# Performance work log

Measured on AMD Instinct MI355X. Metric: run time of the kernel, lower is better.

## Reference

```python
import jax, jax.numpy as jnp
import numpy as np

D_MODEL = 64
NODES = 325
TOPK = 8
HEADS = 4
D_INNER = 2 * D_MODEL      # mamba_ssm default expand=2
D_STATE = 16               # mamba_ssm default
D_CONV = 4                 # mamba_ssm default
DT_RANK = 4                # ceil(d_model/16)
B_SZ, T_LEN = 8, 64
EPS = 1e-5


def _layernorm(x, g, b):
    m = jnp.mean(x, -1, keepdims=True)
    v = jnp.mean(jnp.square(x - m), -1, keepdims=True)
    return (x - m) * jax.lax.rsqrt(v + EPS) * g + b


def _mamba(h, in_proj_w, conv_w, conv_b, x_proj_w, dt_w, dt_b, A_log, D_ssm, out_w):
    # h: (BN, T, D_MODEL)
    BN, T, _ = h.shape
    xz = h @ in_proj_w.T                      # (BN,T,2*di)
    xi, z = jnp.split(xz, 2, axis=-1)
    # depthwise causal conv1d, kernel D_CONV (unrolled: tiny fixed loop)
    xp = jnp.pad(xi, ((0, 0), (D_CONV - 1, 0), (0, 0)))
    xc = conv_b + sum(xp[:, j:j + T, :] * conv_w[:, j] for j in range(D_CONV))
    xc = jax.nn.silu(xc)
    dbl = xc @ x_proj_w.T                     # (BN,T,dt_rank+2*ds)
    dt = dbl[..., :DT_RANK]
    Bc = dbl[..., DT_RANK:DT_RANK + D_STATE]
    Cc = dbl[..., DT_RANK + D_STATE:]
    dt = jax.nn.softplus(dt @ dt_w.T + dt_b)  # (BN,T,di)
    A = -jnp.exp(A_log)                       # (di,ds)

    def step(hs, inp):
        dt_t, B_t, C_t, x_t = inp             # (BN,di),(BN,ds),(BN,ds),(BN,di)
        dA = jnp.exp(dt_t[..., None] * A)     # (BN,di,ds)
        hs = hs * dA + (dt_t * x_t)[..., None] * B_t[:, None, :]
        y = jnp.einsum('bds,bs->bd', hs, C_t)
        return hs, y

    tm = lambda a: jnp.swapaxes(a, 0, 1)      # time-major for scan
    h0 = jnp.zeros((BN, D_INNER, D_STATE), xc.dtype)
    _, ys = jax.lax.scan(step, h0, (tm(dt), tm(Bc), tm(Cc), tm(xc)))
    y = tm(ys) + D_ssm * xc
    y = y * jax.nn.silu(z)
    return y @ out_w.T


def setup_inputs() -> dict:
    key = jax.random.key(0)
    ks = jax.random.split(key, 24)
    rn = lambda k, s, sc=0.05: jax.random.normal(k, s, jnp.float32) * sc
    inp = {}
    inp['x'] = jax.random.normal(ks[0], (B_SZ, T_LEN, NODES, D_MODEL), jnp.float32)
    adj = jax.random.normal(ks[1], (NODES, NODES), jnp.float32)
    _, nbr = jax.lax.top_k(adj, TOPK)
    inp['neighbor_idx'] = nbr.astype(jnp.int32)           # (N, k) static buffer
    # temporal block
    inp['ln1_g'] = jnp.ones((D_MODEL,)); inp['ln1_b'] = jnp.zeros((D_MODEL,))
    inp['in_proj_w'] = rn(ks[2], (2 * D_INNER, D_MODEL))
    inp['conv_w'] = rn(ks[3], (D_INNER, D_CONV), 0.2)
    inp['conv_b'] = jnp.zeros((D_INNER,))
    inp['x_proj_w'] = rn(ks[4], (DT_RANK + 2 * D_STATE, D_INNER))
    inp['dt_w'] = rn(ks[5], (D_INNER, DT_RANK), 0.5)
    inp['dt_b'] = rn(ks[6], (D_INNER,), 0.5)
    inp['A_log'] = jnp.log(jnp.tile(jnp.arange(1, D_STATE + 1, dtype=jnp.float32), (D_INNER, 1)))
    inp['D_ssm'] = jnp.ones((D_INNER,))
    inp['out_w'] = rn(ks[7], (D_MODEL, D_INNER))
    # sparse graph attention
    for nm, k in (('q', 8), ('k', 9), ('v', 10), ('o', 11)):
        inp[nm + '_w'] = rn(ks[k], (D_MODEL, D_MODEL))
        inp[nm + '_b'] = jnp.zeros((D_MODEL,))
    # adaptive gate (final bias init -2.0 per module)
    inp['g1_w'] = rn(ks[12], (D_MODEL // 4, D_MODEL))
    inp['g1_b'] = jnp.zeros((D_MODEL // 4,))
    inp['g2_w'] = rn(ks[13], (1, D_MODEL // 4))
    inp['g2_b'] = jnp.full((1,), -2.0, jnp.float32)
    inp['ln2_g'] = jnp.ones((D_MODEL,)); inp['ln2_b'] = jnp.zeros((D_MODEL,))
    return inp


def reference(x, neighbor_idx, ln1_g, ln1_b, in_proj_w, conv_w, conv_b, x_proj_w,
              dt_w, dt_b, A_log, D_ssm, out_w, q_w, q_b, k_w, k_b, v_w, v_b,
              o_w, o_b, g1_w, g1_b, g2_w, g2_b, ln2_g, ln2_b):
    B, T, N, Dm = x.shape
    # --- temporal Mamba with pre-norm residual (dropout = identity, eval) ---
    xt = x.transpose(0, 2, 1, 3).reshape(B * N, T, Dm)
    xt = xt + _mamba(_layernorm(xt, ln1_g, ln1_b), in_proj_w, conv_w, conv_b,
                     x_proj_w, dt_w, dt_b, A_log, D_ssm, out_w)
    xT = xt.reshape(B, N, T, Dm).transpose(0, 2, 1, 3)     # (B,T,N,D)
    # --- sparse top-k neighbor attention ---
    hd = Dm // HEADS
    Q = (xT @ q_w.T + q_b).reshape(B, T, N, HEADS, hd)
    K = (xT @ k_w.T + k_b).reshape(B, T, N, HEADS, hd)
    V = (xT @ v_w.T + v_b).reshape(B, T, N, HEADS, hd)
    Kn = K[:, :, neighbor_idx]                 # (B,T,N,k,H,hd)
    Vn = V[:, :, neighbor_idx]
    attn = jnp.einsum('btnhd,btnkhd->btnhk', Q, Kn) * (hd ** -0.5)
    attn = jax.nn.softmax(attn, axis=-1)
    og = jnp.einsum('btnhk,btnkhd->btnhd', attn, Vn).reshape(B, T, N, Dm)
    x_graph = og @ o_w.T + o_b
    # --- adaptive gate + fusion + final norm ---
    g = jax.nn.sigmoid(jax.nn.gelu(xT @ g1_w.T + g1_b, approximate=False) @ g2_w.T + g2_b)
    out = xT + g * (x_graph - xT)
    return _layernorm(out, ln2_g, ln2_b)
```

## Files before the change

kernel.cpp:

```cpp
#include <hip/hip_runtime.h>
#include <math.h>

#define NODES   325
#define TOPK    8
#define B_SZ    8
#define T_LEN   64
#define EPS     1e-5f
#define NTOK    ((size_t)B_SZ * T_LEN * NODES)

#define WPAD    132
#define OWPAD   68
#define XCPAD   132
#define DBLPAD  40
#define OFF_H   0
#define OFF_XC  4096
#define OFF_DBL 12544
#define OFF_DTV 15104
#define OFF_W   23296
#define SMEM_BYTES ((23296+8704)*4)

__device__ __forceinline__ float waveSum64(float v){
  #pragma unroll
  for(int m=1;m<64;m<<=1) v += __shfl_xor(v, m, 64);
  return v;
}
__device__ __forceinline__ float groupSum16(float v){
  v += __shfl_xor(v, 1, 64);
  v += __shfl_xor(v, 2, 64);
  v += __shfl_xor(v, 4, 64);
  v += __shfl_xor(v, 8, 64);
  return v;
}
__device__ __forceinline__ float dot64(const float* __restrict__ s,
                                       const float* __restrict__ w, float acc){
  #pragma unroll
  for(int q=0;q<64;q++) acc = fmaf(s[q], w[q], acc);
  return acc;
}
__device__ __forceinline__ float4 f4fma(float s, float4 a, float4 acc){
  acc.x = fmaf(s, a.x, acc.x);
  acc.y = fmaf(s, a.y, acc.y);
  acc.z = fmaf(s, a.z, acc.z);
  acc.w = fmaf(s, a.w, acc.w);
  return acc;
}
__device__ __forceinline__ float dp4(float4 a, float4 b, float acc){
  acc = fmaf(a.x, b.x, acc);
  acc = fmaf(a.y, b.y, acc);
  acc = fmaf(a.z, b.z, acc);
  acc = fmaf(a.w, b.w, acc);
  return acc;
}

__global__ __launch_bounds__(512)
void opt_mamba(const float* __restrict__ x,
               const float* __restrict__ ln1_g, const float* __restrict__ ln1_b,
               const float* __restrict__ in_w,
               const float* __restrict__ conv_w, const float* __restrict__ conv_b,
               const float* __restrict__ xp_w,
               const float* __restrict__ dt_w, const float* __restrict__ dt_b,
               const float* __restrict__ A_log, const float* __restrict__ Dss,
               const float* __restrict__ out_w,
               float* __restrict__ xT)
{
  extern __shared__ float sm[];
  float* s_h   = sm + OFF_H;
  float* s_xc  = sm + OFF_XC;
  float* s_dbl = sm + OFF_DBL;
  float* s_dtv = sm + OFF_DTV;
  float* sW    = sm + OFF_W;

  const int bn   = blockIdx.x;
  const int b    = bn / NODES;
  const int n    = bn % NODES;
  const int tid  = threadIdx.x;
  const int lane = tid & 63;
  const int wv   = tid >> 6;

  const int r0 = (tid & 31) * 4;
  const int t0 = (tid >> 5) * 4;

  for(int idx = tid; idx < 128*64; idx += 512){
    int r = idx >> 6, c = idx & 63;
    sW[c*WPAD + r] = in_w[idx];
  }
  {
    const float g_ln = ln1_g[lane], b_ln = ln1_b[lane];
    #pragma unroll
    for(int i=0;i<8;i++){
      int t = wv*8 + i;
      size_t tok = (size_t)(b*T_LEN + t)*NODES + n;
      float v   = x[tok*64 + lane];
      float m   = waveSum64(v) * (1.f/64.f);
      float c   = v - m;
      float var = waveSum64(c*c) * (1.f/64.f);
      s_h[t*64 + lane] = c * rsqrtf(var + EPS) * g_ln + b_ln;
    }
  }
  __syncthreads();

  {
    float4 acc[4];
    #pragma unroll
    for(int tt=0;tt<4;tt++) acc[tt] = make_float4(0.f,0.f,0.f,0.f);
    for(int c0=0;c0<64;c0+=4){
      float4 w0 = *(const float4*)&sW[(c0+0)*WPAD + r0];
      float4 w1 = *(const float4*)&sW[(c0+1)*WPAD + r0];
      float4 w2 = *(const float4*)&sW[(c0+2)*WPAD + r0];
      float4 w3 = *(const float4*)&sW[(c0+3)*WPAD + r0];
      #pragma unroll
      for(int tt=0;tt<4;tt++){
        float4 h4 = *(const float4*)&s_h[(t0+tt)*64 + c0];
        acc[tt] = f4fma(h4.x, w0, acc[tt]);
        acc[tt] = f4fma(h4.y, w1, acc[tt]);
        acc[tt] = f4fma(h4.z, w2, acc[tt]);
        acc[tt] = f4fma(h4.w, w3, acc[tt]);
      }
    }
    #pragma unroll
    for(int tt=0;tt<4;tt++)
      *(float4*)&s_xc[(t0+tt)*XCPAD + r0] = acc[tt];
  }
  __syncthreads();

  {
    const int dd = tid & 127, tg = tid >> 7;
    float p3 = 0.f, p2 = 0.f, p1 = 0.f;
    if(tg){
      int tq = tg*16;
      p3 = s_xc[(tq-3)*XCPAD + dd];
      p2 = s_xc[(tq-2)*XCPAD + dd];
      p1 = s_xc[(tq-1)*XCPAD + dd];
    }
    __syncthreads();
    const float cw0 = conv_w[dd*4+0], cw1 = conv_w[dd*4+1];
    const float cw2 = conv_w[dd*4+2], cw3 = conv_w[dd*4+3];
    const float cb  = conv_b[dd];
    for(int t=tg*16; t<tg*16+16; t++){
      float xi = s_xc[t*XCPAD + dd];
      float v  = cb + cw0*p3 + cw1*p2 + cw2*p1 + cw3*xi;
      p3 = p2; p2 = p1; p1 = xi;
      s_xc[t*XCPAD + dd] = v / (1.f + __expf(-v));
    }
    for(int idx = tid; idx < 128*64; idx += 512){
      int r = idx >> 6, c = idx & 63;
      sW[c*WPAD + r] = in_w[128*64 + idx];
    }
  }
  __syncthreads();

  float4 zr[4];
  {
    #pragma unroll
    for(int tt=0;tt<4;tt++) zr[tt] = make_float4(0.f,0.f,0.f,0.f);
    for(int c0=0;c0<64;c0+=4){
      float4 w0 = *(const float4*)&sW[(c0+0)*WPAD + r0];
      float4 w1 = *(const float4*)&sW[(c0+1)*WPAD + r0];
      float4 w2 = *(const float4*)&sW[(c0+2)*WPAD + r0];
      float4 w3 = *(const float4*)&sW[(c0+3)*WPAD + r0];
      #pragma unroll
      for(int tt=0;tt<4;tt++){
        float4 h4 = *(const float4*)&s_h[(t0+tt)*64 + c0];
        zr[tt] = f4fma(h4.x, w0, zr[tt]);
        zr[tt] = f4fma(h4.y, w1, zr[tt]);
        zr[tt] = f4fma(h4.z, w2, zr[tt]);
        zr[tt] = f4fma(h4.w, w3, zr[tt]);
      }
    }
  }

  {
    const int td = tid & 63, rg = tid >> 6;
    const int base = rg*5;
    float dacc[5];
    #pragma unroll
    for(int i=0;i<5;i++) dacc[i] = 0.f;
    for(int c0=0;c0<128;c0+=4){
      float4 xc4 = *(const float4*)&s_xc[td*XCPAD + c0];
      #pragma unroll
      for(int i=0;i<5;i++){
        if(base+i < 36){
          float4 w4 = *(const float4*)&xp_w[(base+i)*128 + c0];
          dacc[i] = dp4(xc4, w4, dacc[i]);
        }
      }
    }
    #pragma unroll
    for(int i=0;i<5;i++)
      if(base+i < 36) s_dbl[td*DBLPAD + base + i] = dacc[i];
  }
  __syncthreads();

  {
    const int d = tid & 127, tq = tid >> 7;
    const float dtw0 = dt_w[d*4+0], dtw1 = dt_w[d*4+1];
    const float dtw2 = dt_w[d*4+2], dtw3 = dt_w[d*4+3];
    const float dtb  = dt_b[d];
    #pragma unroll
    for(int j=0;j<16;j++){
      int t = tq + j*4;
      const float* db = &s_dbl[t*DBLPAD];
      float dtv = dtb;
      dtv = fmaf(db[0], dtw0, dtv);
      dtv = fmaf(db[1], dtw1, dtv);
      dtv = fmaf(db[2], dtw2, dtv);
      dtv = fmaf(db[3], dtw3, dtv);
      dtv = fmaxf(dtv, 0.f) + log1pf(__expf(-fabsf(dtv)));
      s_dtv[t*128 + d] = dtv;
    }
  }
  __syncthreads();

  if(tid < 128){
    const int d = tid;
    float A_d[16], hs[16];
    #pragma unroll
    for(int s=0;s<16;s++){ A_d[s] = -__expf(A_log[d*16+s]); hs[s] = 0.f; }
    const float Dd = Dss[d];
    for(int t=0;t<T_LEN;t++){
      const float* db = &s_dbl[t*DBLPAD];
      float dtv = s_dtv[t*128 + d];
      float xc  = s_xc[t*XCPAD + d];
      float dx  = dtv * xc;
      float y   = 0.f;
      #pragma unroll
      for(int s=0;s<16;s++){
        float dA = __expf(dtv * A_d[s]);
        hs[s] = fmaf(dx, db[4+s], hs[s]*dA);
        y     = fmaf(hs[s], db[20+s], y);
      }
      s_xc[t*XCPAD + d] = y + Dd*xc;
    }
  }
  __syncthreads();

  {
    #pragma unroll
    for(int tt=0;tt<4;tt++){
      float4 y4 = *(const float4*)&s_xc[(t0+tt)*XCPAD + r0];
      float4 z4 = zr[tt];
      float4 u;
      u.x = y4.x * (z4.x / (1.f + __expf(-z4.x)));
      u.y = y4.y * (z4.y / (1.f + __expf(-z4.y)));
      u.z = y4.z * (z4.z / (1.f + __expf(-z4.z)));
      u.w = y4.w * (z4.w / (1.f + __expf(-z4.w)));
      *(float4*)&s_xc[(t0+tt)*XCPAD + r0] = u;
    }
    for(int idx = tid; idx < 64*128; idx += 512){
      int j = idx >> 7, c = idx & 127;
      sW[c*OWPAD + j] = out_w[idx];
    }
  }
  __syncthreads();

  {
    const int j0  = (tid & 15) * 4;
    const int t0o = (tid >> 4) * 2;
    float4 oacc[2];
    #pragma unroll
    for(int tt=0;tt<2;tt++) oacc[tt] = make_float4(0.f,0.f,0.f,0.f);
    for(int c0=0;c0<128;c0+=4){
      float4 w0 = *(const float4*)&sW[(c0+0)*OWPAD + j0];
      float4 w1 = *(const float4*)&sW[(c0+1)*OWPAD + j0];
      float4 w2 = *(const float4*)&sW[(c0+2)*OWPAD + j0];
      float4 w3 = *(const float4*)&sW[(c0+3)*OWPAD + j0];
      #pragma unroll
      for(int tt=0;tt<2;tt++){
        float4 u4 = *(const float4*)&s_xc[(t0o+tt)*XCPAD + c0];
        oacc[tt] = f4fma(u4.x, w0, oacc[tt]);
        oacc[tt] = f4fma(u4.y, w1, oacc[tt]);
        oacc[tt] = f4fma(u4.z, w2, oacc[tt]);
        oacc[tt] = f4fma(u4.w, w3, oacc[tt]);
      }
    }
    #pragma unroll
    for(int tt=0;tt<2;tt++){
      int t = t0o + tt;
      size_t tok = (size_t)(b*T_LEN + t)*NODES + n;
      float4 xv = *(const float4*)&x[tok*64 + j0];
      float4 o;
      o.x = xv.x + oacc[tt].x;
      o.y = xv.y + oacc[tt].y;
      o.z = xv.z + oacc[tt].z;
      o.w = xv.w + oacc[tt].w;
      *(float4*)&xT[tok*64 + j0] = o;
    }
  }
}

__global__ __launch_bounds__(256)
void opt_proj(const float* __restrict__ xT,
              const float* __restrict__ k_w, const float* __restrict__ k_b,
              const float* __restrict__ v_w, const float* __restrict__ v_b,
              const float* __restrict__ g1_w, const float* __restrict__ g1_b,
              const float* __restrict__ g2_w, const float* __restrict__ g2_b,
              float* __restrict__ Kb, float* __restrict__ Vb,
              float* __restrict__ gate)
{
  __shared__ float s_x[64*68];
  const int tid = threadIdx.x;
  const size_t tb = (size_t)blockIdx.x * 64;

  for(int i = tid; i < 64*64; i += 256){
    int t = i >> 6, c = i & 63;
    s_x[t*68 + c] = xT[(tb + t)*64 + c];
  }
  __syncthreads();

  const int r0 = (tid & 15) * 4;
  const int t0 = (tid >> 4) * 4;

  {
    float4 b4 = *(const float4*)&k_b[r0];
    float4 acc[4];
    #pragma unroll
    for(int tt=0;tt<4;tt++) acc[tt] = b4;
    for(int c0=0;c0<64;c0+=4){
      float4 w0 = *(const float4*)&k_w[(r0+0)*64 + c0];
      float4 w1 = *(const float4*)&k_w[(r0+1)*64 + c0];
      float4 w2 = *(const float4*)&k_w[(r0+2)*64 + c0];
      float4 w3 = *(const float4*)&k_w[(r0+3)*64 + c0];
      #pragma unroll
      for(int tt=0;tt<4;tt++){
        float4 x4 = *(const float4*)&s_x[(t0+tt)*68 + c0];
        acc[tt].x = dp4(x4, w0, acc[tt].x);
        acc[tt].y = dp4(x4, w1, acc[tt].y);
        acc[tt].z = dp4(x4, w2, acc[tt].z);
        acc[tt].w = dp4(x4, w3, acc[tt].w);
      }
    }
    #pragma unroll
    for(int tt=0;tt<4;tt++)
      *(float4*)&Kb[(tb + t0 + tt)*64 + r0] = acc[tt];
  }

  {
    float4 b4 = *(const float4*)&v_b[r0];
    float4 acc[4];
    #pragma unroll
    for(int tt=0;tt<4;tt++) acc[tt] = b4;
    for(int c0=0;c0<64;c0+=4){
      float4 w0 = *(const float4*)&v_w[(r0+0)*64 + c0];
      float4 w1 = *(const float4*)&v_w[(r0+1)*64 + c0];
      float4 w2 = *(const float4*)&v_w[(r0+2)*64 + c0];
      float4 w3 = *(const float4*)&v_w[(r0+3)*64 + c0];
      #pragma unroll
      for(int tt=0;tt<4;tt++){
        float4 x4 = *(const float4*)&s_x[(t0+tt)*68 + c0];
        acc[tt].x = dp4(x4, w0, acc[tt].x);
        acc[tt].y = dp4(x4, w1, acc[tt].y);
        acc[tt].z = dp4(x4, w2, acc[tt].z);
        acc[tt].w = dp4(x4, w3, acc[tt].w);
      }
    }
    #pragma unroll
    for(int tt=0;tt<4;tt++)
      *(float4*)&Vb[(tb + t0 + tt)*64 + r0] = acc[tt];
  }

  {
    const int td = tid >> 2;
    const int sr = (tid & 3) * 4;
    float partial = 0.f;
    #pragma unroll
    for(int i=0;i<4;i++){
      int r = sr + i;
      float u = dot64(&s_x[td*68], g1_w + r*64, g1_b[r]);
      u = 0.5f * u * (1.f + erff(u * 0.70710678118654752f));
      partial = fmaf(u, g2_w[r], partial);
    }
    partial += __shfl_xor(partial, 1, 64);
    partial += __shfl_xor(partial, 2, 64);
    if((tid & 3) == 0)
      gate[tb + td] = 1.f / (1.f + __expf(-(partial + g2_b[0])));
  }
}

__global__ __launch_bounds__(256)
void opt_attn3(const float* __restrict__ xT,
               const float* __restrict__ Kb, const float* __restrict__ Vb,
               const float* __restrict__ gate, const int* __restrict__ nbr,
               const float* __restrict__ q_w, const float* __restrict__ q_b,
               const float* __restrict__ o_w, const float* __restrict__ o_b,
               const float* __restrict__ ln2_g, const float* __restrict__ ln2_b,
               float* __restrict__ out)
{
  __shared__ float s_x[64*68];
  __shared__ float s_q[64*68];
  const int tid = threadIdx.x;
  const size_t tb = (size_t)blockIdx.x * 64;

  for(int i = tid; i < 64*64; i += 256){
    int t = i >> 6, c = i & 63;
    s_x[t*68 + c] = xT[(tb + t)*64 + c];
  }
  __syncthreads();

  {
    const int r0 = (tid & 15) * 4, t0 = (tid >> 4) * 4;
    float4 b4 = *(const float4*)&q_b[r0];
    float4 acc[4];
    #pragma unroll
    for(int tt=0;tt<4;tt++) acc[tt] = b4;
    for(int c0=0;c0<64;c0+=4){
      float4 w0 = *(const float4*)&q_w[(r0+0)*64 + c0];
      float4 w1 = *(const float4*)&q_w[(r0+1)*64 + c0];
      float4 w2 = *(const float4*)&q_w[(r0+2)*64 + c0];
      float4 w3 = *(const float4*)&q_w[(r0+3)*64 + c0];
      #pragma unroll
      for(int tt=0;tt<4;tt++){
        float4 x4 = *(const float4*)&s_x[(t0+tt)*68 + c0];
        acc[tt].x = dp4(x4, w0, acc[tt].x);
        acc[tt].y = dp4(x4, w1, acc[tt].y);
        acc[tt].z = dp4(x4, w2, acc[tt].z);
        acc[tt].w = dp4(x4, w3, acc[tt].w);
      }
    }
    #pragma unroll
    for(int tt=0;tt<4;tt++)
      *(float4*)&s_q[(t0+tt)*68 + r0] = acc[tt];
  }
  __syncthreads();

  const int td = tid >> 2, h = tid & 3;
  const size_t idxg = tb + td;
  const int n  = (int)(idxg % NODES);
  const int bt = (int)(idxg / NODES);

  const float* qp = &s_q[td*68 + h*16];
  float4 q0 = *(const float4*)(qp+0);
  float4 q1 = *(const float4*)(qp+4);
  float4 q2 = *(const float4*)(qp+8);
  float4 q3 = *(const float4*)(qp+12);
  int rows[TOPK];
  #pragma unroll
  for(int k=0;k<TOPK;k++) rows[k] = bt*NODES + nbr[n*TOPK + k];
  __syncthreads();

  float sc[TOPK];
  #pragma unroll
  for(int k=0;k<TOPK;k++){
    const float* kr = &Kb[(size_t)rows[k]*64 + h*16];
    float4 k0 = *(const float4*)(kr+0);
    float4 k1 = *(const float4*)(kr+4);
    float4 k2 = *(const float4*)(kr+8);
    float4 k3 = *(const float4*)(kr+12);
    float s = dp4(q0,k0, dp4(q1,k1, dp4(q2,k2, dp4(q3,k3, 0.f))));
    sc[k] = s * 0.25f;
  }
  float mx = sc[0];
  #pragma unroll
  for(int k=1;k<TOPK;k++) mx = fmaxf(mx, sc[k]);
  float ssum = 0.f;
  #pragma unroll
  for(int k=0;k<TOPK;k++){ sc[k] = __expf(sc[k]-mx); ssum += sc[k]; }
  float inv = 1.f/ssum;
  float4 o0 = make_float4(0.f,0.f,0.f,0.f), o1 = o0, o2 = o0, o3 = o0;
  #pragma unroll
  for(int k=0;k<TOPK;k++){
    const float* vr = &Vb[(size_t)rows[k]*64 + h*16];
    float p = sc[k]*inv;
    o0 = f4fma(p, *(const float4*)(vr+0),  o0);
    o1 = f4fma(p, *(const float4*)(vr+4),  o1);
    o2 = f4fma(p, *(const float4*)(vr+8),  o2);
    o3 = f4fma(p, *(const float4*)(vr+12), o3);
  }
  {
    float* op = &s_q[td*68 + h*16];
    *(float4*)(op+0)  = o0;
    *(float4*)(op+4)  = o1;
    *(float4*)(op+8)  = o2;
    *(float4*)(op+12) = o3;
  }
  __syncthreads();

  float4 ores[4];
  const int r0 = (tid & 15) * 4, t0 = (tid >> 4) * 4;
  {
    float4 b4 = *(const float4*)&o_b[r0];
    float4 acc[4];
    #pragma unroll
    for(int tt=0;tt<4;tt++) acc[tt] = b4;
    for(int c0=0;c0<64;c0+=4){
      float4 w0 = *(const float4*)&o_w[(r0+0)*64 + c0];
      float4 w1 = *(const float4*)&o_w[(r0+1)*64 + c0];
      float4 w2 = *(const float4*)&o_w[(r0+2)*64 + c0];
      float4 w3 = *(const float4*)&o_w[(r0+3)*64 + c0];
      #pragma unroll
      for(int tt=0;tt<4;tt++){
        float4 g4 = *(const float4*)&s_q[(t0+tt)*68 + c0];
        acc[tt].x = dp4(g4, w0, acc[tt].x);
        acc[tt].y = dp4(g4, w1, acc[tt].y);
        acc[tt].z = dp4(g4, w2, acc[tt].z);
        acc[tt].w = dp4(g4, w3, acc[tt].w);
      }
    }
    #pragma unroll
    for(int tt=0;tt<4;tt++){
      float g = gate[tb + t0 + tt];
      float4 xv = *(const float4*)&s_x[(t0+tt)*68 + r0];
      ores[tt].x = xv.x + g*(acc[tt].x - xv.x);
      ores[tt].y = xv.y + g*(acc[tt].y - xv.y);
      ores[tt].z = xv.z + g*(acc[tt].z - xv.z);
      ores[tt].w = xv.w + g*(acc[tt].w - xv.w);
    }
  }
  __syncthreads();
  #pragma unroll
  for(int tt=0;tt<4;tt++)
    *(float4*)&s_q[(t0+tt)*68 + r0] = ores[tt];
  __syncthreads();

  {
    const float* orow = &s_q[td*68 + h*16];
    float4 a0 = *(const float4*)(orow+0);
    float4 a1 = *(const float4*)(orow+4);
    float4 a2 = *(const float4*)(orow+8);
    float4 a3 = *(const float4*)(orow+12);
    float sum = (a0.x+a0.y+a0.z+a0.w) + (a1.x+a1.y+a1.z+a1.w)
              + (a2.x+a2.y+a2.z+a2.w) + (a3.x+a3.y+a3.z+a3.w);
    sum += __shfl_xor(sum, 1, 64);
    sum += __shfl_xor(sum, 2, 64);
    float mean = sum * (1.f/64.f);
    a0.x-=mean; a0.y-=mean; a0.z-=mean; a0.w-=mean;
    a1.x-=mean; a1.y-=mean; a1.z-=mean; a1.w-=mean;
    a2.x-=mean; a2.y-=mean; a2.z-=mean; a2.w-=mean;
    a3.x-=mean; a3.y-=mean; a3.z-=mean; a3.w-=mean;
    float sq = (a0.x*a0.x+a0.y*a0.y+a0.z*a0.z+a0.w*a0.w)
             + (a1.x*a1.x+a1.y*a1.y+a1.z*a1.z+a1.w*a1.w)
             + (a2.x*a2.x+a2.y*a2.y+a2.z*a2.z+a2.w*a2.w)
             + (a3.x*a3.x+a3.y*a3.y+a3.z*a3.z+a3.w*a3.w);
    sq += __shfl_xor(sq, 1, 64);
    sq += __shfl_xor(sq, 2, 64);
    float rstd = rsqrtf(sq*(1.f/64.f) + EPS);
    float4 g0 = *(const float4*)&ln2_g[h*16+0];
    float4 g1 = *(const float4*)&ln2_g[h*16+4];
    float4 g2 = *(const float4*)&ln2_g[h*16+8];
    float4 g3 = *(const float4*)&ln2_g[h*16+12];
    float4 bb0 = *(const float4*)&ln2_b[h*16+0];
    float4 bb1 = *(const float4*)&ln2_b[h*16+4];
    float4 bb2 = *(const float4*)&ln2_b[h*16+8];
    float4 bb3 = *(const float4*)&ln2_b[h*16+12];
    float* po = &out[idxg*64 + h*16];
    float4 r;
    r.x=a0.x*rstd*g0.x+bb0.x; r.y=a0.y*rstd*g0.y+bb0.y; r.z=a0.z*rstd*g0.z+bb0.z; r.w=a0.w*rstd*g0.w+bb0.w;
    *(float4*)(po+0) = r;
    r.x=a1.x*rstd*g1.x+bb1.x; r.y=a1.y*rstd*g1.y+bb1.y; r.z=a1.z*rstd*g1.z+bb1.z; r.w=a1.w*rstd*g1.w+bb1.w;
    *(float4*)(po+4) = r;
    r.x=a2.x*rstd*g2.x+bb2.x; r.y=a2.y*rstd*g2.y+bb2.y; r.z=a2.z*rstd*g2.z+bb2.z; r.w=a2.w*rstd*g2.w+bb2.w;
    *(float4*)(po+8) = r;
    r.x=a3.x*rstd*g3.x+bb3.x; r.y=a3.y*rstd*g3.y+bb3.y; r.z=a3.z*rstd*g3.z+bb3.z; r.w=a3.w*rstd*g3.w+bb3.w;
    *(float4*)(po+12) = r;
  }
}

__global__ __launch_bounds__(64)
void opt_attn(const float* __restrict__ xT, const int* __restrict__ nbr,
              const float* __restrict__ q_w, const float* __restrict__ q_b,
              const float* __restrict__ k_w, const float* __restrict__ k_b,
              const float* __restrict__ v_w, const float* __restrict__ v_b,
              const float* __restrict__ o_w, const float* __restrict__ o_b,
              const float* __restrict__ g1_w, const float* __restrict__ g1_b,
              const float* __restrict__ g2_w, const float* __restrict__ g2_b,
              const float* __restrict__ ln2_g, const float* __restrict__ ln2_b,
              float* __restrict__ out)
{
  const int idx = blockIdx.x;
  const int n   = idx % NODES;
  const int bt  = idx / NODES;
  const int j   = threadIdx.x;

  __shared__ float s_x[64];
  __shared__ float s_nb[TOPK][64];
  __shared__ float s_og[64];
  __shared__ float s_gate;

  float xv = xT[(size_t)idx*64 + j];
  s_x[j] = xv;
  const int base = bt * NODES;
  #pragma unroll
  for(int k=0;k<TOPK;k++){
    int nb2 = nbr[n*TOPK + k];
    s_nb[k][j] = xT[(size_t)(base + nb2)*64 + j];
  }
  __syncthreads();

  float Qj = dot64(s_x, q_w + j*64, q_b[j]);

  float sc[TOPK], vv[TOPK];
  #pragma unroll
  for(int k=0;k<TOPK;k++){
    float Kk = dot64(s_nb[k], k_w + j*64, k_b[j]);
    vv[k]    = dot64(s_nb[k], v_w + j*64, v_b[j]);
    sc[k]    = groupSum16(Qj * Kk) * 0.25f;
  }
  float m = sc[0];
  #pragma unroll
  for(int k=1;k<TOPK;k++) m = fmaxf(m, sc[k]);
  float ssum = 0.f;
  #pragma unroll
  for(int k=0;k<TOPK;k++){ sc[k] = __expf(sc[k]-m); ssum += sc[k]; }
  float inv = 1.f/ssum;
  float og = 0.f;
  #pragma unroll
  for(int k=0;k<TOPK;k++) og = fmaf(sc[k]*inv, vv[k], og);
  s_og[j] = og;
  __syncthreads();

  float xg = dot64(s_og, o_w + j*64, o_b[j]);

  if(j < 16){
    float u = dot64(s_x, g1_w + j*64, g1_b[j]);
    u = 0.5f * u * (1.f + erff(u * 0.70710678118654752f));
    float contrib = groupSum16(u * g2_w[j]);
    if(j == 0) s_gate = 1.f / (1.f + __expf(-(contrib + g2_b[0])));
  }
  __syncthreads();

  float gg = s_gate;
  float o  = xv + gg * (xg - xv);

  float mm  = waveSum64(o) * (1.f/64.f);
  float c   = o - mm;
  float var = waveSum64(c*c) * (1.f/64.f);
  out[(size_t)idx*64 + j] = c * rsqrtf(var + EPS) * ln2_g[j] + ln2_b[j];
}

extern "C" void kernel_launch(void* const* d_in, const int* in_sizes, int n_in,
                              void* d_out, int out_size, void* d_ws, size_t ws_size,
                              hipStream_t stream)
{
  const float* x      = (const float*)d_in[0];
  const int*   nbr    = (const int*  )d_in[1];
  const float* ln1_g  = (const float*)d_in[2];
  const float* ln1_b  = (const float*)d_in[3];
  const float* in_w   = (const float*)d_in[4];
  const float* conv_w = (const float*)d_in[5];
  const float* conv_b = (const float*)d_in[6];
  const float* xp_w   = (const float*)d_in[7];
  const float* dt_w   = (const float*)d_in[8];
  const float* dt_b   = (const float*)d_in[9];
  const float* A_log  = (const float*)d_in[10];
  const float* Dss    = (const float*)d_in[11];
  const float* out_w  = (const float*)d_in[12];
  const float* q_w    = (const float*)d_in[13];
  const float* q_b    = (const float*)d_in[14];
  const float* k_w    = (const float*)d_in[15];
  const float* k_b    = (const float*)d_in[16];
  const float* v_w    = (const float*)d_in[17];
  const float* v_b    = (const float*)d_in[18];
  const float* o_w    = (const float*)d_in[19];
  const float* o_b    = (const float*)d_in[20];
  const float* g1_w   = (const float*)d_in[21];
  const float* g1_b   = (const float*)d_in[22];
  const float* g2_w   = (const float*)d_in[23];
  const float* g2_b   = (const float*)d_in[24];
  const float* ln2_g  = (const float*)d_in[25];
  const float* ln2_b  = (const float*)d_in[26];

  float* xT   = (float*)d_ws;
  float* Kb   = xT + NTOK*64;
  float* Vb   = Kb + NTOK*64;
  float* gg   = Vb + NTOK*64;
  float* outp = (float*)d_out;

  const size_t need = (NTOK*64*3 + NTOK) * sizeof(float);

  (void)hipFuncSetAttribute(reinterpret_cast<const void*>(opt_mamba),
                            hipFuncAttributeMaxDynamicSharedMemorySize, SMEM_BYTES);

  opt_mamba<<<dim3(B_SZ*NODES), dim3(512), SMEM_BYTES, stream>>>(
      x, ln1_g, ln1_b, in_w, conv_w, conv_b, xp_w, dt_w, dt_b, A_log, Dss, out_w, xT);

  if(ws_size >= need){
    opt_proj<<<dim3((unsigned)(NTOK/64)), dim3(256), 0, stream>>>(
        xT, k_w, k_b, v_w, v_b, g1_w, g1_b, g2_w, g2_b, Kb, Vb, gg);
    opt_attn3<<<dim3((unsigned)(NTOK/64)), dim3(256), 0, stream>>>(
        xT, Kb, Vb, gg, nbr, q_w, q_b, o_w, o_b, ln2_g, ln2_b, outp);
  } else {
    opt_attn<<<dim3((unsigned)NTOK), dim3(64), 0, stream>>>(
        xT, nbr, q_w, q_b, k_w, k_b, v_w, v_b, o_w, o_b,
        g1_w, g1_b, g2_w, g2_b, ln2_g, ln2_b, outp);
  }
}
```

Measured before the change: 1.554 ms.

## Spread selective scan over all 512 threads and fuse dt softplus into scan

The selective scan previously ran on only 128 threads, each holding all 16 state entries, after a separate pass that computed softplus(dt) into shared memory. Now each of the 512 threads handles one channel and 4 states, recomputes dt inline, and reduces the y partials with two xor shuffles. This removes the dt staging buffer and one barrier, and uses all 8 waves for the sequential 64-step loop. In exchange the dt and softplus work is computed four times redundantly, and each step adds shuffles.

```diff
diff --git a/kernel.cpp b/kernel.cpp
--- a/kernel.cpp
+++ b/kernel.cpp
@@ -15,9 +15,8 @@
 #define OFF_H   0
 #define OFF_XC  4096
 #define OFF_DBL 12544
-#define OFF_DTV 15104
-#define OFF_W   23296
-#define SMEM_BYTES ((23296+8704)*4)
+#define OFF_W   15104
+#define SMEM_BYTES (23808*4)
 
 __device__ __forceinline__ float waveSum64(float v){
   #pragma unroll
@@ -67,7 +66,6 @@
   float* s_h   = sm + OFF_H;
   float* s_xc  = sm + OFF_XC;
   float* s_dbl = sm + OFF_DBL;
-  float* s_dtv = sm + OFF_DTV;
   float* sW    = sm + OFF_W;
 
   const int bn   = blockIdx.x;
@@ -192,44 +190,35 @@
   __syncthreads();
 
   {
-    const int d = tid & 127, tq = tid >> 7;
+    const int d  = tid >> 2;
+    const int sq = tid & 3;
+    float A_d[4], hs[4];
+    #pragma unroll
+    for(int i=0;i<4;i++){ A_d[i] = -__expf(A_log[d*16 + sq*4 + i]); hs[i] = 0.f; }
     const float dtw0 = dt_w[d*4+0], dtw1 = dt_w[d*4+1];
     const float dtw2 = dt_w[d*4+2], dtw3 = dt_w[d*4+3];
-    const float dtb  = dt_b[d];
-    #pragma unroll
-    for(int j=0;j<16;j++){
-      int t = tq + j*4;
-      const float* db = &s_dbl[t*DBLPAD];
-      float dtv = dtb;
-      dtv = fmaf(db[0], dtw0, dtv);
-      dtv = fmaf(db[1], dtw1, dtv);
-      dtv = fmaf(db[2], dtw2, dtv);
-      dtv = fmaf(db[3], dtw3, dtv);
-      dtv = fmaxf(dtv, 0.f) + log1pf(__expf(-fabsf(dtv)));
-      s_dtv[t*128 + d] = dtv;
-    }
-  }
-  __syncthreads();
-
-  if(tid < 128){
-    const int d = tid;
-    float A_d[16], hs[16];
-    #pragma unroll
-    for(int s=0;s<16;s++){ A_d[s] = -__expf(A_log[d*16+s]); hs[s] = 0.f; }
-    const float Dd = Dss[d];
+    const float dtb  = dt_b[d], Dd = Dss[d];
     for(int t=0;t<T_LEN;t++){
       const float* db = &s_dbl[t*DBLPAD];
-      float dtv = s_dtv[t*128 + d];
-      float xc  = s_xc[t*XCPAD + d];
-      float dx  = dtv * xc;
-      float y   = 0.f;
-      #pragma unroll
-      for(int s=0;s<16;s++){
-        float dA = __expf(dtv * A_d[s]);
-        hs[s] = fmaf(dx, db[4+s], hs[s]*dA);
-        y     = fmaf(hs[s], db[20+s], y);
-      }
-      s_xc[t*XCPAD + d] = y + Dd*xc;
+      float4 dt4 = *(const float4*)db;
+      float dtv = dtb;
+      dtv = fmaf(dt4.x, dtw0, dtv);
+      dtv = fmaf(dt4.y, dtw1, dtv);
+      dtv = fmaf(dt4.z, dtw2, dtv);
+      dtv = fmaf(dt4.w, dtw3, dtv);
+      dtv = fmaxf(dtv, 0.f) + log1pf(__expf(-fabsf(dtv)));
+      float xc = s_xc[t*XCPAD + d];
+      float dx = dtv * xc;
+      float4 Bv = *(const float4*)&db[4  + sq*4];
+      float4 Cv = *(const float4*)&db[20 + sq*4];
+      float yp = 0.f;
+      hs[0] = fmaf(dx, Bv.x, hs[0]*__expf(dtv*A_d[0])); yp = fmaf(hs[0], Cv.x, yp);
+      hs[1] = fmaf(dx, Bv.y, hs[1]*__expf(dtv*A_d[1])); yp = fmaf(hs[1], Cv.y, yp);
+      hs[2] = fmaf(dx, Bv.z, hs[2]*__expf(dtv*A_d[2])); yp = fmaf(hs[2], Cv.z, yp);
+      hs[3] = fmaf(dx, Bv.w, hs[3]*__expf(dtv*A_d[3])); yp = fmaf(hs[3], Cv.w, yp);
+      yp += __shfl_xor(yp, 1, 64);
+      yp += __shfl_xor(yp, 2, 64);
+      if(sq == 0) s_xc[t*XCPAD + d] = yp + Dd*xc;
     }
   }
   __syncthreads();
```

Result: slower. 1.635 ms (+5.2%).
